# Performance work log

Measured on AMD Instinct MI355X. Metric: run time of the kernel, lower is better.

Reference implementation:

```python
import jax, jax.numpy as jnp
import numpy as np

E, S, H, D, B = 8, 64, 2048, 1024, 8192
LN_EPS = 1e-5


def setup_inputs() -> dict:
    key = jax.random.key(0)
    ks = jax.random.split(key, 12)
    n = lambda k, shape: jax.random.normal(k, shape, jnp.float32) * 0.02
    return {
        "raw_state": jax.random.normal(ks[0], (B, S), jnp.float32),
        "has_proprio": jax.random.randint(ks[1], (B,), 0, 2, jnp.int32),
        "expert_idx": jax.random.randint(ks[2], (B,), 0, E, jnp.int32),
        "pw1": n(ks[3], (E, S, H)), "pb1": jnp.zeros((E, H), jnp.float32),
        "pw2": n(ks[4], (E, H, D)), "pb2": jnp.zeros((E, D), jnp.float32),
        "qw1": n(ks[5], (E, S, H)), "qb1": jnp.zeros((E, H), jnp.float32),
        "qw2": n(ks[6], (E, H, D)), "qb2": jnp.zeros((E, D), jnp.float32),
        "ln_g": jnp.ones((E, D), jnp.float32), "ln_b": jnp.zeros((E, D), jnp.float32),
        "tw1": n(ks[7], (E, D, H)), "tb1": jnp.zeros((E, H), jnp.float32),
        "tw2": n(ks[8], (E, H, D)), "tb2": jnp.zeros((E, D), jnp.float32),
    }


def _gelu(x):
    # torch nn.GELU default = exact erf form
    return jax.nn.gelu(x, approximate=False)


def _expert_fwd(x, sel, w):
    (pw1, pb1, pw2, pb2, qw1, qb1, qw2, qb2, ln_g, ln_b, tw1, tb1, tw2, tb2) = w
    placeholder = _gelu(x @ pw1 + pb1) @ pw2 + pb2      # [B, D]
    proprio = _gelu(x @ qw1 + qb1) @ qw2 + qb2          # [B, D]
    mixed = placeholder * (1.0 - sel) + proprio * sel    # [B, D]
    mu = jnp.mean(mixed, axis=-1, keepdims=True)
    var = jnp.mean(jnp.square(mixed - mu), axis=-1, keepdims=True)
    normed = (mixed - mu) * jax.lax.rsqrt(var + LN_EPS) * ln_g + ln_b
    return _gelu(normed @ tw1 + tb1) @ tw2 + tb2         # [B, D]


def reference(raw_state, has_proprio, expert_idx,
              pw1, pb1, pw2, pb2, qw1, qb1, qw2, qb2,
              ln_g, ln_b, tw1, tb1, tw2, tb2):
    sel = has_proprio.astype(raw_state.dtype)[:, None]  # [B, 1]
    n_experts = pw1.shape[0]
    acc = jnp.zeros((raw_state.shape[0], tw2.shape[-1]), raw_state.dtype)
    # Fixed small loop over experts; rows routed via mask-select (same math
    # as the original index_select -> projector -> index_copy_).
    for e in range(n_experts):
        w = (pw1[e], pb1[e], pw2[e], pb2[e], qw1[e], qb1[e], qw2[e], qb2[e],
             ln_g[e], ln_b[e], tw1[e], tb1[e], tw2[e], tb2[e])
        oe = _expert_fwd(raw_state, sel, w)
        acc = jnp.where((expert_idx == e)[:, None], oe, acc)
    return acc[:, None, :]  # [B, 1, D]
```

## Files before the change

### kernel.cpp

```cpp
#include <hip/hip_runtime.h>
#include <math.h>

typedef unsigned short u16;
typedef unsigned int   u32;
typedef __attribute__((ext_vector_type(8))) short bh8;
typedef __attribute__((ext_vector_type(4))) float f4;

#define TM 128
#define TN 128
#define TK 32

__device__ __forceinline__ u16 f2b(float f) {
  u32 u = __builtin_bit_cast(u32, f);
  u += 0x7fffu + ((u >> 16) & 1u);
  return (u16)(u >> 16);
}
__device__ __forceinline__ float gelu_f(float x) {
  return 0.5f * x * (1.0f + erff(x * 0.70710678118654752f));
}

__device__ __forceinline__ void gl2lds16(const u16* g, u16* l) {
  __builtin_amdgcn_global_load_lds(
      (const __attribute__((address_space(1))) u32*)g,
      (__attribute__((address_space(3))) u32*)l, 16, 0, 0);
}

__global__ __launch_bounds__(128) void init_routing(int* __restrict__ R) {
  R[threadIdx.x] = 0;
}

__global__ __launch_bounds__(256) void hist_kernel(const int* __restrict__ eidx,
                                                   const int* __restrict__ hasp,
                                                   int* __restrict__ R,
                                                   int* __restrict__ grp) {
  int t = blockIdx.x * 256 + threadIdx.x;
  int g = eidx[t] * 2 + (hasp[t] != 0 ? 1 : 0);
  grp[t] = g;
  atomicAdd(&R[g], 1);
}

__global__ __launch_bounds__(64) void scan_kernel(int* __restrict__ R) {
  if (threadIdx.x == 0) {
    int* cnt = R; int* cur = R + 16; int* gs = R + 32; int* to = R + 64;
    gs[0] = 0; to[0] = 0;
    for (int g = 0; g < 16; g++) {
      gs[g + 1] = gs[g] + cnt[g];
      cur[g] = gs[g];
      to[g + 1] = to[g] + (cnt[g] + TM - 1) / TM;
    }
  }
}

__global__ __launch_bounds__(256) void scatter_kernel(const int* __restrict__ grp,
                                                      int* __restrict__ R,
                                                      int* __restrict__ perm) {
  int t = blockIdx.x * 256 + threadIdx.x;
  int g = grp[t];
  int pos = atomicAdd(&R[16 + g], 1);
  perm[pos] = t;
}

__global__ __launch_bounds__(256) void gather_kernel(const float* __restrict__ raw,
                                                     const int* __restrict__ perm,
                                                     u16* __restrict__ Xg) {
  int t = blockIdx.x * 256 + threadIdx.x;
  int pos = t >> 6, ln = t & 63;
  int orig = perm[pos];
  Xg[(size_t)pos * 64 + ln] = f2b(raw[(size_t)orig * 64 + ln]);
}

__global__ __launch_bounds__(256) void transpose_cvt(const float* __restrict__ srcP,
                                                     const float* __restrict__ srcQ,
                                                     int twoSrc, int Rr, int Cc,
                                                     u16* __restrict__ dst) {
  int m = blockIdx.z;
  const float* src = twoSrc ? (((m & 1) ? srcQ : srcP) + (size_t)(m >> 1) * Rr * Cc)
                            : (srcP + (size_t)m * Rr * Cc);
  u16* d = dst + (size_t)m * Rr * Cc;
  __shared__ u16 t[64][66];
  int c0 = blockIdx.x * 64, r0 = blockIdx.y * 64;
  int tx = threadIdx.x, ty = threadIdx.y;
#pragma unroll
  for (int i = 0; i < 16; i++) {
    int r = ty + i * 4;
    t[tx][r] = f2b(src[(size_t)(r0 + r) * Cc + c0 + tx]);
  }
  __syncthreads();
#pragma unroll
  for (int i = 0; i < 16; i++) {
    int c = ty + i * 4;
    d[(size_t)(c0 + c) * Rr + r0 + tx] = t[c][tx];
  }
}

__global__ __launch_bounds__(256)
void gemm_grouped(const u16* __restrict__ A, int lda,
                  const u16* __restrict__ W, int wShift, int K, int N,
                  const float* __restrict__ biasP, const float* __restrict__ biasQ,
                  int branchBias, int doGelu,
                  u16* __restrict__ outB, float* __restrict__ outF,
                  int doScatter, int ldo,
                  const int* __restrict__ gstart, const int* __restrict__ tileOff,
                  const int* __restrict__ perm) {
  __shared__ __align__(16) u16 As[TM * TK];
  __shared__ __align__(16) u16 Bs[TN * TK];

  int bidM = blockIdx.x;
  int tot = tileOff[16];
  if (bidM >= tot) return;
  int g = 0;
  while (g < 15 && bidM >= tileOff[g + 1]) g++;
  int rowStart = gstart[g] + (bidM - tileOff[g]) * TM;
  int rowEnd = gstart[g + 1];

  const u16* Wg = W + (size_t)(g >> wShift) * N * K;
  int e = g >> 1;
  const float* bias = ((branchBias && (g & 1)) ? biasQ : biasP) + (size_t)e * N;

  int tid = threadIdx.x;
  int lane = tid & 63;
  int wv = tid >> 6;
  int wm = (wv >> 1) * 64, wn = (wv & 1) * 64;
  int l15 = lane & 15, l4 = lane >> 4;
  int colBase = blockIdx.y * TN;

  int cA = wv * 2;
  int rA0 = cA * 16 + (lane >> 2);
  int rA1 = rA0 + 16;
  int kq8 = (lane & 3) * 8;
  int grA0 = rowStart + rA0; grA0 = grA0 < rowEnd ? grA0 : (rowEnd - 1);
  int grA1 = rowStart + rA1; grA1 = grA1 < rowEnd ? grA1 : (rowEnd - 1);
  const u16* aSrc0 = A + (size_t)grA0 * lda + kq8;
  const u16* aSrc1 = A + (size_t)grA1 * lda + kq8;
  const u16* bSrc0 = Wg + (size_t)(colBase + rA0) * K + kq8;
  const u16* bSrc1 = Wg + (size_t)(colBase + rA1) * K + kq8;
  u16* aDst0 = &As[cA * 512];
  u16* aDst1 = &As[cA * 512 + 512];
  u16* bDst0 = &Bs[cA * 512];
  u16* bDst1 = &Bs[cA * 512 + 512];

  f4 acc[4][4];
#pragma unroll
  for (int i = 0; i < 4; i++)
#pragma unroll
    for (int j = 0; j < 4; j++) acc[i][j] = (f4){0.f, 0.f, 0.f, 0.f};

  for (int k0 = 0; k0 < K; k0 += TK) {
    __syncthreads();
    gl2lds16(aSrc0 + k0, aDst0);
    gl2lds16(aSrc1 + k0, aDst1);
    gl2lds16(bSrc0 + k0, bDst0);
    gl2lds16(bSrc1 + k0, bDst1);
    __syncthreads();

    bh8 a[4], b[4];
#pragma unroll
    for (int i = 0; i < 4; i++)
      a[i] = *reinterpret_cast<const bh8*>(&As[(wm + i * 16 + l15) * TK + l4 * 8]);
#pragma unroll
    for (int j = 0; j < 4; j++)
      b[j] = *reinterpret_cast<const bh8*>(&Bs[(wn + j * 16 + l15) * TK + l4 * 8]);
#pragma unroll
    for (int i = 0; i < 4; i++)
#pragma unroll
      for (int j = 0; j < 4; j++)
        acc[i][j] = __builtin_amdgcn_mfma_f32_16x16x32_bf16(a[i], b[j], acc[i][j], 0, 0, 0);
  }

#pragma unroll
  for (int i = 0; i < 4; i++) {
#pragma unroll
    for (int r = 0; r < 4; r++) {
      int row = rowStart + wm + i * 16 + l4 * 4 + r;
      if (row < rowEnd) {
        int orow = doScatter ? perm[row] : row;
#pragma unroll
        for (int j = 0; j < 4; j++) {
          int col = colBase + wn + j * 16 + l15;
          float v = acc[i][j][r] + bias[col];
          if (doGelu) v = gelu_f(v);
          if (outF) outF[(size_t)orow * ldo + col] = v;
          else      outB[(size_t)orow * ldo + col] = f2b(v);
        }
      }
    }
  }
}

__global__ __launch_bounds__(256) void ln_kernel(const float* __restrict__ MIX,
                                                 u16* __restrict__ NRM,
                                                 const float* __restrict__ lng,
                                                 const float* __restrict__ lnb,
                                                 const int* __restrict__ gstart) {
  const int D = 1024;
  int pos = blockIdx.x;
  int g = 0;
  while (g < 15 && pos >= gstart[g + 1]) g++;
  int e = g >> 1;
  int tid = threadIdx.x;
  float x[4];
  float s = 0.f, s2 = 0.f;
#pragma unroll
  for (int i = 0; i < 4; i++) {
    float v = MIX[(size_t)pos * D + tid + i * 256];
    x[i] = v; s += v; s2 += v * v;
  }
#pragma unroll
  for (int off = 32; off >= 1; off >>= 1) {
    s += __shfl_down(s, off);
    s2 += __shfl_down(s2, off);
  }
  __shared__ float red[8];
  int wv = tid >> 6;
  if ((tid & 63) == 0) { red[wv] = s; red[4 + wv] = s2; }
  __syncthreads();
  if (tid == 0) {
    red[0] = red[0] + red[1] + red[2] + red[3];
    red[4] = red[4] + red[5] + red[6] + red[7];
  }
  __syncthreads();
  float mean = red[0] / D;
  float var = red[4] / D - mean * mean;
  float rstd = rsqrtf(var + 1e-5f);
#pragma unroll
  for (int i = 0; i < 4; i++) {
    int c = tid + i * 256;
    float v = (x[i] - mean) * rstd * lng[(size_t)e * D + c] + lnb[(size_t)e * D + c];
    NRM[(size_t)pos * D + c] = f2b(v);
  }
}

extern "C" void kernel_launch(void* const* d_in, const int* in_sizes, int n_in,
                              void* d_out, int out_size, void* d_ws, size_t ws_size,
                              hipStream_t stream) {
  const float* raw = (const float*)d_in[0];
  const int* hasp = (const int*)d_in[1];
  const int* eidx = (const int*)d_in[2];
  const float* pw1 = (const float*)d_in[3];  const float* pb1 = (const float*)d_in[4];
  const float* pw2 = (const float*)d_in[5];  const float* pb2 = (const float*)d_in[6];
  const float* qw1 = (const float*)d_in[7];  const float* qb1 = (const float*)d_in[8];
  const float* qw2 = (const float*)d_in[9];  const float* qb2 = (const float*)d_in[10];
  const float* lng = (const float*)d_in[11]; const float* lnb = (const float*)d_in[12];
  const float* tw1 = (const float*)d_in[13]; const float* tb1 = (const float*)d_in[14];
  const float* tw2 = (const float*)d_in[15]; const float* tb2 = (const float*)d_in[16];
  float* out = (float*)d_out;

  const int B = in_sizes[0] / 64;
  const int S = 64, H = 2048, D = 1024, E = 8;

  char* ws = (char*)d_ws;
  size_t o = 0;
  int* R    = (int*)(ws + o); o += 1024;
  int* grp  = (int*)(ws + o); o += (size_t)B * 4;
  int* perm = (int*)(ws + o); o += (size_t)B * 4;
  u16* Xg   = (u16*)(ws + o); o += (size_t)B * S * 2;
  u16* Hbuf = (u16*)(ws + o); o += (size_t)B * H * 2;
  float* MIX = (float*)(ws + o); o += (size_t)B * D * 4;
  u16* NRM  = (u16*)(ws + o); o += (size_t)B * D * 2;
  u16* W1T  = (u16*)(ws + o); o += (size_t)2 * E * S * H * 2;
  u16* WB   = (u16*)(ws + o);
  u16* T1T  = WB;
  u16* T2T  = WB + (size_t)E * D * H;

  int* gstart = R + 32;
  int* toff = R + 64;

  init_routing<<<1, 128, 0, stream>>>(R);
  hist_kernel<<<B / 256, 256, 0, stream>>>(eidx, hasp, R, grp);
  scan_kernel<<<1, 64, 0, stream>>>(R);
  scatter_kernel<<<B / 256, 256, 0, stream>>>(grp, R, perm);
  gather_kernel<<<B / 4, 256, 0, stream>>>(raw, perm, Xg);

  dim3 tb(64, 4);
  transpose_cvt<<<dim3(H / 64, S / 64, 16), tb, 0, stream>>>(pw1, qw1, 1, S, H, W1T);
  transpose_cvt<<<dim3(D / 64, H / 64, 16), tb, 0, stream>>>(pw2, qw2, 1, H, D, WB);

  const int maxT = B / TM + 16;
  gemm_grouped<<<dim3(maxT, H / TN), 256, 0, stream>>>(
      Xg, S, W1T, 0, S, H, pb1, qb1, 1, 1, Hbuf, nullptr, 0, H, gstart, toff, perm);
  gemm_grouped<<<dim3(maxT, D / TN), 256, 0, stream>>>(
      Hbuf, H, WB, 0, H, D, pb2, qb2, 1, 0, nullptr, MIX, 0, D, gstart, toff, perm);
  ln_kernel<<<B, 256, 0, stream>>>(MIX, NRM, lng, lnb, gstart);
  transpose_cvt<<<dim3(H / 64, D / 64, 8), tb, 0, stream>>>(tw1, nullptr, 0, D, H, T1T);
  transpose_cvt<<<dim3(D / 64, H / 64, 8), tb, 0, stream>>>(tw2, nullptr, 0, H, D, T2T);
  gemm_grouped<<<dim3(maxT, H / TN), 256, 0, stream>>>(
      NRM, D, T1T, 1, D, H, tb1, nullptr, 0, 1, Hbuf, nullptr, 0, H, gstart, toff, perm);
  gemm_grouped<<<dim3(maxT, D / TN), 256, 0, stream>>>(
      Hbuf, H, T2T, 1, H, D, tb2, nullptr, 0, 0, nullptr, out, 1, D, gstart, toff, perm);
}
```

Before: 653.0 us.

## Double-buffer LDS tiles in grouped GEMM and halve the M tile

The grouped GEMM now ping-pongs between two LDS buffers. It issues the global-to-LDS loads for the next K slice before computing on the current one, and needs only one barrier per iteration. The M tile drops from 128 to 64 rows, giving each wave a 32x64 sub-tile, and launch bounds request 4 blocks per CU. The goal is to hide global load latency and raise occupancy, at the cost of less A/B reuse per MFMA and more blocks re-reading weights.

```diff
diff --git a/kernel.cpp b/kernel.cpp
--- a/kernel.cpp
+++ b/kernel.cpp
@@ -6,7 +6,7 @@
 typedef __attribute__((ext_vector_type(8))) short bh8;
 typedef __attribute__((ext_vector_type(4))) float f4;
 
-#define TM 128
+#define TM 64
 #define TN 128
 #define TK 32
 
@@ -93,7 +93,7 @@
   }
 }
 
-__global__ __launch_bounds__(256)
+__global__ __launch_bounds__(256, 4)
 void gemm_grouped(const u16* __restrict__ A, int lda,
                   const u16* __restrict__ W, int wShift, int K, int N,
                   const float* __restrict__ biasP, const float* __restrict__ biasQ,
@@ -102,8 +102,8 @@
                   int doScatter, int ldo,
                   const int* __restrict__ gstart, const int* __restrict__ tileOff,
                   const int* __restrict__ perm) {
-  __shared__ __align__(16) u16 As[TM * TK];
-  __shared__ __align__(16) u16 Bs[TN * TK];
+  __shared__ __align__(16) u16 As[2][TM * TK];
+  __shared__ __align__(16) u16 Bs[2][TN * TK];
 
   int bidM = blockIdx.x;
   int tot = tileOff[16];
@@ -120,63 +120,63 @@
   int tid = threadIdx.x;
   int lane = tid & 63;
   int wv = tid >> 6;
-  int wm = (wv >> 1) * 64, wn = (wv & 1) * 64;
+  int wvM = (wv >> 1) * 32, wvN = (wv & 1) * 64;
   int l15 = lane & 15, l4 = lane >> 4;
   int colBase = blockIdx.y * TN;
 
-  int cA = wv * 2;
-  int rA0 = cA * 16 + (lane >> 2);
-  int rA1 = rA0 + 16;
-  int kq8 = (lane & 3) * 8;
-  int grA0 = rowStart + rA0; grA0 = grA0 < rowEnd ? grA0 : (rowEnd - 1);
-  int grA1 = rowStart + rA1; grA1 = grA1 < rowEnd ? grA1 : (rowEnd - 1);
-  const u16* aSrc0 = A + (size_t)grA0 * lda + kq8;
-  const u16* aSrc1 = A + (size_t)grA1 * lda + kq8;
-  const u16* bSrc0 = Wg + (size_t)(colBase + rA0) * K + kq8;
-  const u16* bSrc1 = Wg + (size_t)(colBase + rA1) * K + kq8;
-  u16* aDst0 = &As[cA * 512];
-  u16* aDst1 = &As[cA * 512 + 512];
-  u16* bDst0 = &Bs[cA * 512];
-  u16* bDst1 = &Bs[cA * 512 + 512];
-
-  f4 acc[4][4];
-#pragma unroll
-  for (int i = 0; i < 4; i++)
+  int sr = tid >> 2;
+  int kq8 = (tid & 3) * 8;
+  int grA = rowStart + sr; grA = grA < rowEnd ? grA : (rowEnd - 1);
+  const u16* aSrc  = A + (size_t)grA * lda + kq8;
+  const u16* bSrc0 = Wg + (size_t)(colBase + sr) * K + kq8;
+  const u16* bSrc1 = Wg + (size_t)(colBase + 64 + sr) * K + kq8;
+
+  f4 acc[2][4];
+#pragma unroll
+  for (int i = 0; i < 2; i++)
 #pragma unroll
     for (int j = 0; j < 4; j++) acc[i][j] = (f4){0.f, 0.f, 0.f, 0.f};
 
-  for (int k0 = 0; k0 < K; k0 += TK) {
+  int nk = K / TK;
+  gl2lds16(aSrc, &As[0][tid * 8]);
+  gl2lds16(bSrc0, &Bs[0][tid * 8]);
+  gl2lds16(bSrc1, &Bs[0][2048 + tid * 8]);
+
+  for (int kt = 0; kt < nk; kt++) {
     __syncthreads();
-    gl2lds16(aSrc0 + k0, aDst0);
-    gl2lds16(aSrc1 + k0, aDst1);
-    gl2lds16(bSrc0 + k0, bDst0);
-    gl2lds16(bSrc1 + k0, bDst1);
-    __syncthreads();
-
-    bh8 a[4], b[4];
-#pragma unroll
-    for (int i = 0; i < 4; i++)
-      a[i] = *reinterpret_cast<const bh8*>(&As[(wm + i * 16 + l15) * TK + l4 * 8]);
+    if (kt + 1 < nk) {
+      int k0 = (kt + 1) * TK;
+      int b = (kt + 1) & 1;
+      gl2lds16(aSrc + k0, &As[b][tid * 8]);
+      gl2lds16(bSrc0 + k0, &Bs[b][tid * 8]);
+      gl2lds16(bSrc1 + k0, &Bs[b][2048 + tid * 8]);
+    }
+    const u16* Asb = As[kt & 1];
+    const u16* Bsb = Bs[kt & 1];
+    bh8 a[2], b[4];
+#pragma unroll
+    for (int i = 0; i < 2; i++)
+      a[i] = *reinterpret_cast<const bh8*>(&Asb[(wvM + i * 16 + l15) * TK + l4 * 8]);
 #pragma unroll
     for (int j = 0; j < 4; j++)
-      b[j] = *reinterpret_cast<const bh8*>(&Bs[(wn + j * 16 + l15) * TK + l4 * 8]);
-#pragma unroll
-    for (int i = 0; i < 4; i++)
+      b[j] = *reinterpret_cast<const bh8*>(&Bsb[(wvN + j * 16 + l15) * TK + l4 * 8]);
+#pragma unroll
+    for (int i = 0; i < 2; i++)
 #pragma unroll
       for (int j = 0; j < 4; j++)
         acc[i][j] = __builtin_amdgcn_mfma_f32_16x16x32_bf16(a[i], b[j], acc[i][j], 0, 0, 0);
   }
 
 #pragma unroll
-  for (int i = 0; i < 4; i++) {
+  for (int i = 0; i < 2; i++) {
 #pragma unroll
     for (int r = 0; r < 4; r++) {
-      int row = rowStart + wm + i * 16 + l4 * 4 + r;
+      int row = rowStart + wvM + i * 16 + l4 * 4 + r;
       if (row < rowEnd) {
         int orow = doScatter ? perm[row] : row;
 #pragma unroll
         for (int j = 0; j < 4; j++) {
-          int col = colBase + wn + j * 16 + l15;
+          int col = colBase + wvN + j * 16 + l15;
           float v = acc[i][j][r] + bias[col];
           if (doGelu) v = gelu_f(v);
           if (outF) outF[(size_t)orow * ldo + col] = v;
```

Result: slower. 670.1 us (+2.6%).
